# Kernel tuning notes

Measured on AMD Instinct MI355X. Metric: run time of the kernel, lower is better.

The kernel has to match this reference:

```python
import jax, jax.numpy as jnp
import numpy as np

N, E, B, IN, H = 20000, 50000, 1024, 32, 64

def setup_inputs() -> dict:
    key = jax.random.key(0)
    ks = jax.random.split(key, 32)
    d = {}
    d["x"] = jax.random.normal(ks[0], (N, IN), jnp.float32)
    d["edge_index"] = jax.random.randint(ks[1], (2, E), 0, N)
    d["edge_attr"] = jax.random.uniform(ks[2], (E, 6), dtype=jnp.float32)
    d["batch"] = jnp.sort(jax.random.randint(ks[3], (N,), 0, B))
    d["t"] = jax.random.uniform(ks[4], (B, 1), dtype=jnp.float32)
    d["p"] = jax.random.uniform(ks[5], (B, 1), dtype=jnp.float32)
    d["num_graphs"] = B
    def lin(k, fan_in, shape):
        return jax.random.normal(k, shape, jnp.float32) * (1.0 / np.sqrt(fan_in))
    # lin0: IN -> H
    d["W0"] = lin(ks[6], IN, (IN, H)); d["b0"] = jnp.zeros((H,), jnp.float32)
    # edge MLP: 6 -> 64 -> H*H
    d["We1"] = lin(ks[7], 6, (6, 64)); d["be1"] = jnp.zeros((64,), jnp.float32)
    d["We2"] = lin(ks[8], 64, (64, H * H)); d["be2"] = jnp.zeros((H * H,), jnp.float32)
    # NNConv root weight + bias
    d["Wroot"] = lin(ks[9], H, (H, H)); d["bconv"] = jnp.zeros((H,), jnp.float32)
    # GRU (input H, hidden H), torch layout [3H, *] gate order r,z,n
    d["gru_wih"] = lin(ks[10], H, (3 * H, H)); d["gru_whh"] = lin(ks[11], H, (3 * H, H))
    d["gru_bih"] = jnp.zeros((3 * H,), jnp.float32); d["gru_bhh"] = jnp.zeros((3 * H,), jnp.float32)
    # Set2Set LSTM (input 2H, hidden H), torch layout [4H, *] gate order i,f,g,o
    d["l_wih"] = lin(ks[12], 2 * H, (4 * H, 2 * H)); d["l_whh"] = lin(ks[13], H, (4 * H, H))
    d["l_bih"] = jnp.zeros((4 * H,), jnp.float32); d["l_bhh"] = jnp.zeros((4 * H,), jnp.float32)
    # readout MLP
    d["W1"] = lin(ks[14], 2 * H + 2, (2 * H + 2, H)); d["b1"] = jnp.zeros((H,), jnp.float32)
    d["W2"] = lin(ks[15], H, (H, 64)); d["b2"] = jnp.zeros((64,), jnp.float32)
    d["W3"] = lin(ks[16], 64, (64, 1)); d["b3"] = jnp.zeros((1,), jnp.float32)
    return d


def reference(x, edge_attr, t, p, W0, b0, We1, be1, We2, be2, Wroot, bconv,
              gru_wih, gru_whh, gru_bih, gru_bhh, l_wih, l_whh, l_bih, l_bhh,
              W1, b1, W2, b2, W3, b3, edge_index, batch, num_graphs):
    n_nodes = x.shape[0]
    hdim = W0.shape[1]
    src, dst = edge_index[0], edge_index[1]

    out = jax.nn.relu(x @ W0 + b0)            # [N,H]
    h = out

    # edge MLP -> per-edge weight matrices [E,H,H] (edge_attr is loop-invariant)
    ew = (jax.nn.relu(edge_attr @ We1 + be1) @ We2 + be2).reshape(-1, hdim, hdim)

    for _ in range(4):
        # NNConv: gather source features, per-edge matmul, scatter-add to targets
        msg = jnp.einsum('eh,eho->eo', out[src], ew)                 # [E,H]
        agg = jax.ops.segment_sum(msg, dst, num_segments=n_nodes)    # [N,H]
        m = jax.nn.relu(agg + out @ Wroot + bconv)
        # GRU step (single timestep)
        gi = m @ gru_wih.T + gru_bih
        gh = h @ gru_whh.T + gru_bhh
        ir, iz, inn = jnp.split(gi, 3, axis=-1)
        hr, hz, hn = jnp.split(gh, 3, axis=-1)
        r = jax.nn.sigmoid(ir + hr)
        z = jax.nn.sigmoid(iz + hz)
        nn_ = jnp.tanh(inn + r * hn)
        h = (1.0 - z) * nn_ + z * h
        out = h

    # Set2Set pooling, 3 processing steps
    qh = jnp.zeros((num_graphs, hdim), x.dtype)
    qc = jnp.zeros((num_graphs, hdim), x.dtype)
    q_star = jnp.zeros((num_graphs, 2 * hdim), x.dtype)
    for _ in range(3):
        g = q_star @ l_wih.T + l_bih + qh @ l_whh.T + l_bhh
        gi_, gf_, gg_, go_ = jnp.split(g, 4, axis=-1)
        qc = jax.nn.sigmoid(gf_) * qc + jax.nn.sigmoid(gi_) * jnp.tanh(gg_)
        qh = jax.nn.sigmoid(go_) * jnp.tanh(qc)
        q = qh                                                        # [B,H]
        e = jnp.sum(out * q[batch], axis=-1, keepdims=True)          # [N,1]
        emax = jax.ops.segment_max(e, batch, num_segments=num_graphs)
        a = jnp.exp(e - emax[batch])
        asum = jax.ops.segment_sum(a, batch, num_segments=num_graphs)
        a = a / asum[batch]                                           # segment softmax
        r_ = jax.ops.segment_sum(a * out, batch, num_segments=num_graphs)
        q_star = jnp.concatenate([q, r_], axis=-1)

    feat = jnp.concatenate([q_star, t, p], axis=-1)                   # [B,2H+2]
    y = jax.nn.relu(feat @ W1 + b1)
    y = jax.nn.relu(y @ W2 + b2)
    y = y @ W3 + b3
    return y.reshape(-1)
```

## Files before the change

### kernel.cpp

```cpp
#include <hip/hip_runtime.h>
#include <math.h>

#define N_NODES 20000
#define N_EDGES 50000
#define NB      1024
#define IND     32
#define HDIM    64

typedef __attribute__((ext_vector_type(8))) short bf16x8;
typedef __attribute__((ext_vector_type(4))) float f32x4;

static inline size_t align_up(size_t x, size_t a) { return (x + a - 1) & ~(a - 1); }

__device__ __forceinline__ float sigmoidf_(float x) {
    return 1.0f / (1.0f + __expf(-x));
}
__device__ __forceinline__ float tanhf_(float x) {
    float xc = fminf(fmaxf(x, -15.0f), 15.0f);
    float e = __expf(2.0f * xc);
    return (e - 1.0f) / (e + 1.0f);
}
__device__ __forceinline__ unsigned pk2(float p0, float p1) {
    unsigned u0 = __float_as_uint(p0) + 0x8000u;
    unsigned u1 = __float_as_uint(p1) + 0x8000u;
    return __builtin_amdgcn_perm(u1, u0, 0x07060302u);
}
__device__ __forceinline__ unsigned bf1(float v) {
    return (__float_as_uint(v) + 0x8000u) >> 16;
}

__global__ void k_transpose(const float* __restrict__ in, float* __restrict__ out, int R, int C) {
    int idx = blockIdx.x * 256 + threadIdx.x;
    if (idx >= R * C) return;
    int r = idx / C, c = idx - r * C;
    out[c * R + r] = in[idx];
}

__global__ void k_we2b(const float* __restrict__ We2, const float* __restrict__ be2,
                       short* __restrict__ We2b) {
    int idx = blockIdx.x * 256 + threadIdx.x;
    int s = idx >> 12;
    int col = idx & 4095;
    int k = col >> 6, o = col & 63;
    float val = (s < 64) ? We2[k * 4096 + s * 64 + o] : be2[k * 64 + o];
    int dst = s * 4096 + (((o >> 4) * 128 + (k >> 5) * 64 + ((k >> 3) & 3) * 16 + (o & 15)) << 3) + (k & 7);
    We2b[dst] = (short)bf1(val);
}

__global__ void k_wsplit(const float* __restrict__ Wroot, const float* __restrict__ gwhh,
                         const float* __restrict__ gwih,
                         short* __restrict__ WB1h, short* __restrict__ WB1l,
                         short* __restrict__ WB2h, short* __restrict__ WB2l) {
    int idx = blockIdx.x * 256 + threadIdx.x;
    if (idx >= 28672) return;
    bool b1 = idx < 16384;
    int li = b1 ? idx : idx - 16384;
    int j = li & 7, lane = (li >> 3) & 63, c = (li >> 9) & 1, otile = li >> 10;
    int k = c * 32 + (lane >> 4) * 8 + j;
    int o = otile * 16 + (lane & 15);
    float val;
    if (b1) val = (o < 64) ? Wroot[k * 64 + o] : gwhh[(o - 64) * 64 + k];
    else    val = gwih[o * 64 + k];
    unsigned hs = bf1(val);
    float lo = val - __uint_as_float(hs << 16);
    unsigned ls = bf1(lo);
    if (b1) { WB1h[li] = (short)hs; WB1l[li] = (short)ls; }
    else    { WB2h[li] = (short)hs; WB2l[li] = (short)ls; }
}

__global__ void k_offsets(const int* __restrict__ batch, int* __restrict__ offs) {
    int i = blockIdx.x * 256 + threadIdx.x;
    if (i > NB) return;
    int lo = 0, hi = N_NODES;
    while (lo < hi) { int mid = (lo + hi) >> 1; if (batch[mid] < i) lo = mid + 1; else hi = mid; }
    offs[i] = lo;
}

__global__ void k_count(const int* __restrict__ ei, int* __restrict__ deg) {
    int e = blockIdx.x * 256 + threadIdx.x;
    if (e < N_EDGES) atomicAdd(&deg[ei[N_EDGES + e]], 1);
}

__global__ void k_scan(const int* __restrict__ deg, int* __restrict__ rowptr, int* __restrict__ cursor) {
    __shared__ int s_w[16];
    int t = threadIdx.x;
    int base = t * 20;
    int v[20]; int s = 0;
#pragma unroll
    for (int i = 0; i < 20; ++i) {
        int idx = base + i;
        v[i] = (idx < N_NODES) ? deg[idx] : 0;
        s += v[i];
    }
    int lane = t & 63, w = t >> 6;
    int inc = s;
#pragma unroll
    for (int off = 1; off < 64; off <<= 1) {
        int o = __shfl_up(inc, off);
        if (lane >= off) inc += o;
    }
    if (lane == 63) s_w[w] = inc;
    __syncthreads();
    if (w == 0 && lane < 16) {
        int x = s_w[lane];
        int xs = x;
#pragma unroll
        for (int off = 1; off < 16; off <<= 1) {
            int o = __shfl_up(xs, off);
            if (lane >= off) xs += o;
        }
        s_w[lane] = xs - x;
    }
    __syncthreads();
    int run = s_w[w] + (inc - s);
#pragma unroll
    for (int i = 0; i < 20; ++i) {
        int idx = base + i;
        if (idx < N_NODES) { rowptr[idx] = run; cursor[idx] = run; }
        else if (idx == N_NODES) rowptr[idx] = run;
        run += v[i];
    }
}

__global__ void k_fill(const int* __restrict__ ei, int* __restrict__ cursor, int* __restrict__ perm) {
    int e = blockIdx.x * 256 + threadIdx.x;
    if (e < N_EDGES) {
        int pos = atomicAdd(&cursor[ei[N_EDGES + e]], 1);
        perm[pos] = e;
    }
}

__global__ void k_node_init(const float* __restrict__ x, const float* __restrict__ W0,
                            const float* __restrict__ b0, float* __restrict__ hbuf) {
    int tid = threadIdx.x;
    int w = tid >> 6, j = tid & 63;
    int n = blockIdx.x * 4 + w;
    float acc = b0[j];
    const float* xr = x + n * IND;
#pragma unroll
    for (int i = 0; i < IND; ++i) acc = fmaf(xr[i], W0[i * 64 + j], acc);
    hbuf[n * 64 + j] = fmaxf(acc, 0.0f);
}

__global__ void k_edge_feat(const float* __restrict__ ea, const float* __restrict__ We1,
                            const float* __restrict__ be1, float* __restrict__ re) {
    int tid = threadIdx.x;
    int w = tid >> 6, k = tid & 63;
    int e = blockIdx.x * 4 + w;
    if (e >= N_EDGES) return;
    float acc = be1[k];
    const float* er = ea + e * 6;
#pragma unroll
    for (int i = 0; i < 6; ++i) acc = fmaf(er[i], We1[i * 64 + k], acc);
    re[e * 64 + k] = fmaxf(acc, 0.0f);
}

__launch_bounds__(256, 3)
__global__ void k_msg_mfma(const float* __restrict__ hbuf, const float* __restrict__ reb,
                           const short* __restrict__ We2b, const int* __restrict__ ei,
                           float* __restrict__ msg) {
    __shared__ float s_v[64][64];
    int tid = threadIdx.x;
    int eb = blockIdx.x * 64;
    int lane = tid & 63;
    int w = tid >> 6;
    int l15 = lane & 15, lhi = lane >> 4;

    {
        int se = tid >> 2;
        int sh = tid & 3;
        int ge = eb + se;
        const float* rowp = (ge < N_EDGES) ? (hbuf + (size_t)ei[ge] * 64) : (const float*)0;
#pragma unroll
        for (int rr4 = 0; rr4 < 4; ++rr4) {
            int hb = rr4 * 16 + sh * 4;
            float4 vv = rowp ? *(const float4*)(rowp + hb) : make_float4(0.f, 0.f, 0.f, 0.f);
            s_v[hb + 0][se] = vv.x; s_v[hb + 1][se] = vv.y;
            s_v[hb + 2][se] = vv.z; s_v[hb + 3][se] = vv.w;
        }
    }

    union U { int4 i4; bf16x8 v; };
    U a_re[4][2];
#pragma unroll
    for (int m = 0; m < 4; ++m) {
        int ge = eb + m * 16 + l15;
        if (ge < N_EDGES) {
            const float* rp = reb + (size_t)ge * 64 + lhi * 8;
            float4 x0 = *(const float4*)(rp);
            float4 x1 = *(const float4*)(rp + 4);
            float4 y0 = *(const float4*)(rp + 32);
            float4 y1 = *(const float4*)(rp + 36);
            a_re[m][0].i4 = make_int4(pk2(x0.x, x0.y), pk2(x0.z, x0.w), pk2(x1.x, x1.y), pk2(x1.z, x1.w));
            a_re[m][1].i4 = make_int4(pk2(y0.x, y0.y), pk2(y0.z, y0.w), pk2(y1.x, y1.y), pk2(y1.z, y1.w));
        } else {
            a_re[m][0].i4 = make_int4(0, 0, 0, 0);
            a_re[m][1].i4 = make_int4(0, 0, 0, 0);
        }
    }

    const int4* bp0 = (const int4*)We2b + (w * 128 + lane);
    const int4* bp1 = bp0 + 64;
    int4 Sc0[4], Sc1[4];
#pragma unroll
    for (int j = 0; j < 4; ++j) {
        Sc0[j] = bp0[j * 512];
        Sc1[j] = bp1[j * 512];
    }

    __syncthreads();

    const f32x4 zero4 = {0.f, 0.f, 0.f, 0.f};
    f32x4 macc[4];
#pragma unroll
    for (int m = 0; m < 4; ++m) macc[m] = zero4;

    float4 vv[4], vn[4];
#pragma unroll
    for (int m = 0; m < 4; ++m) vv[m] = *(const float4*)&s_v[0][m * 16 + lhi * 4];

    for (int g = 0; g < 16; ++g) {
#pragma unroll
        for (int j = 0; j < 4; ++j) {
            int s = g * 4 + j;
            int snext = (s < 63) ? (s + 1) : 63;
#pragma unroll
            for (int m = 0; m < 4; ++m)
                vn[m] = *(const float4*)&s_v[snext][m * 16 + lhi * 4];
            U bb0, bb1; bb0.i4 = Sc0[j]; bb1.i4 = Sc1[j];
#pragma unroll
            for (int m = 0; m < 4; ++m) {
                f32x4 t = __builtin_amdgcn_mfma_f32_16x16x32_bf16(a_re[m][0].v, bb0.v, zero4, 0, 0, 0);
                t = __builtin_amdgcn_mfma_f32_16x16x32_bf16(a_re[m][1].v, bb1.v, t, 0, 0, 0);
                macc[m][0] = fmaf(vv[m].x, t[0], macc[m][0]);
                macc[m][1] = fmaf(vv[m].y, t[1], macc[m][1]);
                macc[m][2] = fmaf(vv[m].z, t[2], macc[m][2]);
                macc[m][3] = fmaf(vv[m].w, t[3], macc[m][3]);
            }
            int sload = (s + 4 <= 64) ? (s + 4) : 64;
            Sc0[j] = bp0[sload * 512];
            Sc1[j] = bp1[sload * 512];
#pragma unroll
            for (int m = 0; m < 4; ++m) vv[m] = vn[m];
        }
    }

    {
        U bb0, bb1; bb0.i4 = Sc0[0]; bb1.i4 = Sc1[0];
#pragma unroll
        for (int m = 0; m < 4; ++m) {
            int e = m * 16 + l15;
            U a0, a1;
            a0.i4 = make_int4(
                pk2(s_v[lhi * 8 + 0][e], s_v[lhi * 8 + 1][e]),
                pk2(s_v[lhi * 8 + 2][e], s_v[lhi * 8 + 3][e]),
                pk2(s_v[lhi * 8 + 4][e], s_v[lhi * 8 + 5][e]),
                pk2(s_v[lhi * 8 + 6][e], s_v[lhi * 8 + 7][e]));
            a1.i4 = make_int4(
                pk2(s_v[32 + lhi * 8 + 0][e], s_v[32 + lhi * 8 + 1][e]),
                pk2(s_v[32 + lhi * 8 + 2][e], s_v[32 + lhi * 8 + 3][e]),
                pk2(s_v[32 + lhi * 8 + 4][e], s_v[32 + lhi * 8 + 5][e]),
                pk2(s_v[32 + lhi * 8 + 6][e], s_v[32 + lhi * 8 + 7][e]));
            macc[m] = __builtin_amdgcn_mfma_f32_16x16x32_bf16(a0.v, bb0.v, macc[m], 0, 0, 0);
            macc[m] = __builtin_amdgcn_mfma_f32_16x16x32_bf16(a1.v, bb1.v, macc[m], 0, 0, 0);
        }
    }
    int o = w * 16 + l15;
#pragma unroll
    for (int m = 0; m < 4; ++m) {
#pragma unroll
        for (int r = 0; r < 4; ++r) {
            int el = m * 16 + lhi * 4 + r;
            int ge = eb + el;
            if (ge < N_EDGES) msg[(size_t)ge * 64 + o] = macc[m][r];
        }
    }
}

__launch_bounds__(256, 2)
__global__ void k_node_update(float* __restrict__ hbuf, const float* __restrict__ msg,
                              const int* __restrict__ rowptr, const int* __restrict__ perm,
                              const short* __restrict__ WB1h, const short* __restrict__ WB1l,
                              const short* __restrict__ WB2h, const short* __restrict__ WB2l,
                              const float* __restrict__ bconv, const float* __restrict__ bih,
                              const float* __restrict__ bhh) {
    __shared__ short s_hh[64][72];
    __shared__ short s_hl[64][72];
    __shared__ short s_mh[64][72];
    __shared__ short s_ml[64][72];
    __shared__ float s_agg[64][68];
    int tid = threadIdx.x;
    int nbase = blockIdx.x * 64;
    int lane = tid & 63, w = tid >> 6;
    int l15 = lane & 15, lhi = lane >> 4;

    {
        int nt = tid >> 2, q = tid & 3;
        int n = nbase + nt;
        bool valid = n < N_NODES;
#pragma unroll
        for (int c4 = 0; c4 < 4; ++c4) {
            int col = q * 16 + c4 * 4;
            float4 v = valid ? *(const float4*)&hbuf[(size_t)n * 64 + col]
                             : make_float4(0.f, 0.f, 0.f, 0.f);
            unsigned h01 = pk2(v.x, v.y), h23 = pk2(v.z, v.w);
            float f0 = __uint_as_float(h01 << 16);
            float f1 = __uint_as_float(h01 & 0xffff0000u);
            float f2 = __uint_as_float(h23 << 16);
            float f3 = __uint_as_float(h23 & 0xffff0000u);
            unsigned l01 = pk2(v.x - f0, v.y - f1), l23 = pk2(v.z - f2, v.w - f3);
            *(unsigned*)&s_hh[nt][col]     = h01;
            *(unsigned*)&s_hh[nt][col + 2] = h23;
            *(unsigned*)&s_hl[nt][col]     = l01;
            *(unsigned*)&s_hl[nt][col + 2] = l23;
        }
        float4 aggv[4];
#pragma unroll
        for (int c4 = 0; c4 < 4; ++c4)
            aggv[c4] = valid ? *(const float4*)&bconv[q * 16 + c4 * 4]
                             : make_float4(0.f, 0.f, 0.f, 0.f);
        if (valid) {
            int rs = rowptr[n], rend = rowptr[n + 1];
            for (int qq = rs; qq < rend; ++qq) {
                const float* mrow = msg + (size_t)perm[qq] * 64 + q * 16;
#pragma unroll
                for (int c4 = 0; c4 < 4; ++c4) {
                    float4 mv = *(const float4*)&mrow[c4 * 4];
                    aggv[c4].x += mv.x; aggv[c4].y += mv.y;
                    aggv[c4].z += mv.z; aggv[c4].w += mv.w;
                }
            }
        }
#pragma unroll
        for (int c4 = 0; c4 < 4; ++c4)
            *(float4*)&s_agg[nt][q * 16 + c4 * 4] = aggv[c4];
    }
    __syncthreads();

    union U { int4 i4; bf16x8 v; };
    U ah[4][2], al[4][2];
#pragma unroll
    for (int m = 0; m < 4; ++m)
#pragma unroll
        for (int c = 0; c < 2; ++c) {
            ah[m][c].i4 = *(const int4*)&s_hh[m * 16 + l15][c * 32 + lhi * 8];
            al[m][c].i4 = *(const int4*)&s_hl[m * 16 + l15][c * 32 + lhi * 8];
        }

    const int4* B1h = (const int4*)WB1h;
    const int4* B1l = (const int4*)WB1l;
    const int4* B2h = (const int4*)WB2h;
    const int4* B2l = (const int4*)WB2l;

    f32x4 C0[4], G[3][4], I[3][4];

    {
        int ot = w;
        U bh0, bh1, bl0, bl1;
        bh0.i4 = B1h[(ot * 2 + 0) * 64 + lane];
        bh1.i4 = B1h[(ot * 2 + 1) * 64 + lane];
        bl0.i4 = B1l[(ot * 2 + 0) * 64 + lane];
        bl1.i4 = B1l[(ot * 2 + 1) * 64 + lane];
#pragma unroll
        for (int m = 0; m < 4; ++m) {
            f32x4 c;
#pragma unroll
            for (int r = 0; r < 4; ++r) c[r] = s_agg[m * 16 + lhi * 4 + r][w * 16 + l15];
            c = __builtin_amdgcn_mfma_f32_16x16x32_bf16(ah[m][0].v, bh0.v, c, 0, 0, 0);
            c = __builtin_amdgcn_mfma_f32_16x16x32_bf16(ah[m][1].v, bh1.v, c, 0, 0, 0);
            c = __builtin_amdgcn_mfma_f32_16x16x32_bf16(al[m][0].v, bh0.v, c, 0, 0, 0);
            c = __builtin_amdgcn_mfma_f32_16x16x32_bf16(al[m][1].v, bh1.v, c, 0, 0, 0);
            c = __builtin_amdgcn_mfma_f32_16x16x32_bf16(ah[m][0].v, bl0.v, c, 0, 0, 0);
            c = __builtin_amdgcn_mfma_f32_16x16x32_bf16(ah[m][1].v, bl1.v, c, 0, 0, 0);
            C0[m] = c;
        }
    }
#pragma unroll
    for (int m = 0; m < 4; ++m)
#pragma unroll
        for (int r = 0; r < 4; ++r) {
            float mv = fmaxf(C0[m][r], 0.0f);
            int row = m * 16 + lhi * 4 + r, col = w * 16 + l15;
            unsigned hs = bf1(mv);
            float lof = mv - __uint_as_float(hs << 16);
            s_mh[row][col] = (short)hs;
            s_ml[row][col] = (short)bf1(lof);
        }
#pragma unroll
    for (int p = 1; p < 4; ++p) {
        int ot = p * 4 + w;
        U bh0, bh1, bl0, bl1;
        bh0.i4 = B1h[(ot * 2 + 0) * 64 + lane];
        bh1.i4 = B1h[(ot * 2 + 1) * 64 + lane];
        bl0.i4 = B1l[(ot * 2 + 0) * 64 + lane];
        bl1.i4 = B1l[(ot * 2 + 1) * 64 + lane];
        float bv = bhh[(p - 1) * 64 + w * 16 + l15];
#pragma unroll
        for (int m = 0; m < 4; ++m) {
            f32x4 c = {bv, bv, bv, bv};
            c = __builtin_amdgcn_mfma_f32_16x16x32_bf16(ah[m][0].v, bh0.v, c, 0, 0, 0);
            c = __builtin_amdgcn_mfma_f32_16x16x32_bf16(ah[m][1].v, bh1.v, c, 0, 0, 0);
            c = __builtin_amdgcn_mfma_f32_16x16x32_bf16(al[m][0].v, bh0.v, c, 0, 0, 0);
            c = __builtin_amdgcn_mfma_f32_16x16x32_bf16(al[m][1].v, bh1.v, c, 0, 0, 0);
            c = __builtin_amdgcn_mfma_f32_16x16x32_bf16(ah[m][0].v, bl0.v, c, 0, 0, 0);
            c = __builtin_amdgcn_mfma_f32_16x16x32_bf16(ah[m][1].v, bl1.v, c, 0, 0, 0);
            G[p - 1][m] = c;
        }
    }
    __syncthreads();
    U mh[4][2], ml[4][2];
#pragma unroll
    for (int m = 0; m < 4; ++m)
#pragma unroll
        for (int c = 0; c < 2; ++c) {
            mh[m][c].i4 = *(const int4*)&s_mh[m * 16 + l15][c * 32 + lhi * 8];
            ml[m][c].i4 = *(const int4*)&s_ml[m * 16 + l15][c * 32 + lhi * 8];
        }
#pragma unroll
    for (int p = 0; p < 3; ++p) {
        int ot = p * 4 + w;
        U bh0, bh1, bl0, bl1;
        bh0.i4 = B2h[(ot * 2 + 0) * 64 + lane];
        bh1.i4 = B2h[(ot * 2 + 1) * 64 + lane];
        bl0.i4 = B2l[(ot * 2 + 0) * 64 + lane];
        bl1.i4 = B2l[(ot * 2 + 1) * 64 + lane];
        float bv = bih[p * 64 + w * 16 + l15];
#pragma unroll
        for (int m = 0; m < 4; ++m) {
            f32x4 c = {bv, bv, bv, bv};
            c = __builtin_amdgcn_mfma_f32_16x16x32_bf16(mh[m][0].v, bh0.v, c, 0, 0, 0);
            c = __builtin_amdgcn_mfma_f32_16x16x32_bf16(mh[m][1].v, bh1.v, c, 0, 0, 0);
            c = __builtin_amdgcn_mfma_f32_16x16x32_bf16(ml[m][0].v, bh0.v, c, 0, 0, 0);
            c = __builtin_amdgcn_mfma_f32_16x16x32_bf16(ml[m][1].v, bh1.v, c, 0, 0, 0);
            c = __builtin_amdgcn_mfma_f32_16x16x32_bf16(mh[m][0].v, bl0.v, c, 0, 0, 0);
            c = __builtin_amdgcn_mfma_f32_16x16x32_bf16(mh[m][1].v, bl1.v, c, 0, 0, 0);
            I[p][m] = c;
        }
    }
#pragma unroll
    for (int m = 0; m < 4; ++m)
#pragma unroll
        for (int r = 0; r < 4; ++r) {
            int row = m * 16 + lhi * 4 + r;
            int n = nbase + row;
            if (n < N_NODES) {
                int col = w * 16 + l15;
                float hold = __uint_as_float(((unsigned)(unsigned short)s_hh[row][col]) << 16)
                           + __uint_as_float(((unsigned)(unsigned short)s_hl[row][col]) << 16);
                float rg = sigmoidf_(I[0][m][r] + G[0][m][r]);
                float z  = sigmoidf_(I[1][m][r] + G[1][m][r]);
                float nn = tanhf_(I[2][m][r] + rg * G[2][m][r]);
                hbuf[(size_t)n * 64 + col] = (1.0f - z) * nn + z * hold;
            }
        }
}

__global__ void k_lstm(const float* __restrict__ q_star, float* __restrict__ qh, float* __restrict__ qc,
                       const float* __restrict__ l_wihT, const float* __restrict__ l_whhT,
                       const float* __restrict__ l_bih, const float* __restrict__ l_bhh) {
    __shared__ float s_qs[128];
    __shared__ float s_qh[64];
    __shared__ float s_g[256];
    int b = blockIdx.x;
    int j = threadIdx.x;
    if (j < 128) s_qs[j] = q_star[b * 128 + j];
    else if (j < 192) s_qh[j - 128] = qh[b * 64 + (j - 128)];
    __syncthreads();
    float g = l_bih[j] + l_bhh[j];
#pragma unroll 8
    for (int i = 0; i < 128; ++i) g = fmaf(s_qs[i], l_wihT[i * 256 + j], g);
#pragma unroll 8
    for (int i = 0; i < 64; ++i)  g = fmaf(s_qh[i], l_whhT[i * 256 + j], g);
    s_g[j] = g;
    __syncthreads();
    if (j < 64) {
        float ci = sigmoidf_(s_g[j]);
        float cf = sigmoidf_(s_g[64 + j]);
        float cg = tanhf_(s_g[128 + j]);
        float co = sigmoidf_(s_g[192 + j]);
        float c = cf * qc[b * 64 + j] + ci * cg;
        qc[b * 64 + j] = c;
        qh[b * 64 + j] = co * tanhf_(c);
    }
}

__global__ void k_attention(const float* __restrict__ hbuf, const float* __restrict__ qh,
                            const int* __restrict__ offs, float* __restrict__ q_star) {
    int tid = threadIdx.x;
    int w = tid >> 6, lane = tid & 63;
    int b = blockIdx.x * 4 + w;
    int s = offs[b], e = offs[b + 1];
    float qv = qh[b * 64 + lane];
    float mx = -1e30f, l = 0.0f, racc = 0.0f;
    for (int n = s; n < e; ++n) {
        float xv = hbuf[n * 64 + lane];
        float prod = xv * qv;
#pragma unroll
        for (int off = 32; off > 0; off >>= 1) prod += __shfl_xor(prod, off);
        float mnew = fmaxf(mx, prod);
        float scale = __expf(mx - mnew);
        float wgt = __expf(prod - mnew);
        l = l * scale + wgt;
        racc = racc * scale + wgt * xv;
        mx = mnew;
    }
    float r = (e > s) ? (racc / l) : 0.0f;
    q_star[b * 128 + lane] = qv;
    q_star[b * 128 + 64 + lane] = r;
}

__global__ void k_readout(const float* __restrict__ q_star, const float* __restrict__ t,
                          const float* __restrict__ p, const float* __restrict__ W1,
                          const float* __restrict__ b1, const float* __restrict__ W2,
                          const float* __restrict__ b2, const float* __restrict__ W3,
                          const float* __restrict__ b3, float* __restrict__ y) {
    __shared__ float s_qs[4][128];
    __shared__ float s_y[4][64];
    int tid = threadIdx.x;
    int w = tid >> 6, j = tid & 63;
    int b = blockIdx.x * 4 + w;
    s_qs[w][j] = q_star[b * 128 + j];
    s_qs[w][64 + j] = q_star[b * 128 + 64 + j];
    __syncthreads();
    float acc = b1[j];
#pragma unroll 8
    for (int i = 0; i < 128; ++i) acc = fmaf(s_qs[w][i], W1[i * 64 + j], acc);
    acc = fmaf(t[b], W1[128 * 64 + j], acc);
    acc = fmaf(p[b], W1[129 * 64 + j], acc);
    acc = fmaxf(acc, 0.0f);
    s_y[w][j] = acc;
    __syncthreads();
    float acc2 = b2[j];
#pragma unroll 8
    for (int i = 0; i < 64; ++i) acc2 = fmaf(s_y[w][i], W2[i * 64 + j], acc2);
    acc2 = fmaxf(acc2, 0.0f);
    float part = acc2 * W3[j];
#pragma unroll
    for (int off = 32; off > 0; off >>= 1) part += __shfl_xor(part, off);
    if (j == 0) y[b] = part + b3[0];
}

extern "C" void kernel_launch(void* const* d_in, const int* in_sizes, int n_in,
                              void* d_out, int out_size, void* d_ws, size_t ws_size,
                              hipStream_t stream) {
    const float* x     = (const float*)d_in[0];
    const int*   ei    = (const int*)  d_in[1];
    const float* ea    = (const float*)d_in[2];
    const int*   batch = (const int*)  d_in[3];
    const float* t     = (const float*)d_in[4];
    const float* p     = (const float*)d_in[5];
    const float* W0    = (const float*)d_in[7];
    const float* b0    = (const float*)d_in[8];
    const float* We1   = (const float*)d_in[9];
    const float* be1   = (const float*)d_in[10];
    const float* We2   = (const float*)d_in[11];
    const float* be2   = (const float*)d_in[12];
    const float* Wroot = (const float*)d_in[13];
    const float* bconv = (const float*)d_in[14];
    const float* gwih  = (const float*)d_in[15];
    const float* gwhh  = (const float*)d_in[16];
    const float* gbih  = (const float*)d_in[17];
    const float* gbhh  = (const float*)d_in[18];
    const float* lwih  = (const float*)d_in[19];
    const float* lwhh  = (const float*)d_in[20];
    const float* lbih  = (const float*)d_in[21];
    const float* lbhh  = (const float*)d_in[22];
    const float* W1    = (const float*)d_in[23];
    const float* b1    = (const float*)d_in[24];
    const float* W2    = (const float*)d_in[25];
    const float* b2    = (const float*)d_in[26];
    const float* W3    = (const float*)d_in[27];
    const float* b3    = (const float*)d_in[28];
    float* y = (float*)d_out;

    char* ws = (char*)d_ws;
    size_t off = 0;
    auto alloc = [&](size_t nbytes) {
        void* ptr = (void*)(ws + off);
        off += align_up(nbytes, 256);
        return ptr;
    };
    float* hbuf   = (float*)alloc((size_t)N_NODES * 64 * 4);
    float* reb    = (float*)alloc((size_t)N_EDGES * 64 * 4);
    float* msg    = (float*)alloc((size_t)N_EDGES * 64 * 4);
    short* We2b   = (short*)alloc((size_t)65 * 4096 * 2);
    short* WB1h   = (short*)alloc(16384 * 2);
    short* WB1l   = (short*)alloc(16384 * 2);
    short* WB2h   = (short*)alloc(12288 * 2);
    short* WB2l   = (short*)alloc(12288 * 2);
    float* lwihT  = (float*)alloc(128 * 256 * 4);
    float* lwhhT  = (float*)alloc(64 * 256 * 4);
    float* qh     = (float*)alloc(NB * 64 * 4);
    float* qc     = (float*)alloc(NB * 64 * 4);
    float* qstar  = (float*)alloc(NB * 128 * 4);
    int*   offs   = (int*)  alloc((NB + 1) * 4);
    int*   deg    = (int*)  alloc(N_NODES * 4);
    int*   rowptr = (int*)  alloc((N_NODES + 1) * 4);
    int*   cursor = (int*)  alloc(N_NODES * 4);
    int*   perm   = (int*)  alloc(N_EDGES * 4);

    k_transpose<<<(256 * 128 + 255) / 256, 256, 0, stream>>>(lwih, lwihT, 256, 128);
    k_transpose<<<(256 * 64 + 255) / 256, 256, 0, stream>>>(lwhh, lwhhT, 256, 64);
    k_we2b<<<65 * 4096 / 256, 256, 0, stream>>>(We2, be2, We2b);
    k_wsplit<<<(28672 + 255) / 256, 256, 0, stream>>>(Wroot, gwhh, gwih, WB1h, WB1l, WB2h, WB2l);
    k_offsets<<<5, 256, 0, stream>>>(batch, offs);
    hipMemsetAsync(qh, 0, (size_t)(NB * 64 + NB * 64 + NB * 128) * 4, stream);
    hipMemsetAsync(deg, 0, (size_t)N_NODES * 4, stream);
    k_count<<<(N_EDGES + 255) / 256, 256, 0, stream>>>(ei, deg);
    k_scan<<<1, 1024, 0, stream>>>(deg, rowptr, cursor);
    k_fill<<<(N_EDGES + 255) / 256, 256, 0, stream>>>(ei, cursor, perm);

    k_node_init<<<N_NODES / 4, 256, 0, stream>>>(x, W0, b0, hbuf);
    k_edge_feat<<<N_EDGES / 4, 256, 0, stream>>>(ea, We1, be1, reb);

    for (int it = 0; it < 4; ++it) {
        k_msg_mfma<<<(N_EDGES + 63) / 64, 256, 0, stream>>>(hbuf, reb, We2b, ei, msg);
        k_node_update<<<(N_NODES + 63) / 64, 256, 0, stream>>>(hbuf, msg, rowptr, perm,
                                                               WB1h, WB1l, WB2h, WB2l,
                                                               bconv, gbih, gbhh);
    }

    for (int itr = 0; itr < 3; ++itr) {
        k_lstm<<<NB, 256, 0, stream>>>(qstar, qh, qc, lwihT, lwhhT, lbih, lbhh);
        k_attention<<<NB / 4, 256, 0, stream>>>(hbuf, qh, offs, qstar);
    }

    k_readout<<<NB / 4, 256, 0, stream>>>(qstar, t, p, W1, b1, W2, b2, W3, b3, y);
}
```

Baseline: 490.7 us.

## Fuse prep, init and Set2Set kernels; widen message kernel to 128 edges

The weight-prep, transpose and offset kernels are merged into one launch, and the node-init and edge-feature kernels into another. The three LSTM/attention rounds and the readout become a single per-graph kernel that keeps the LSTM state in registers, so the qh, qc and q_star buffers and their memset go away. The message MFMA kernel now uses 512 threads covering 128 edges per block, with two edge halves sharing output tiles and a shorter weight prefetch depth. The aim is fewer launches and less global traffic, at the cost of a serial per-graph Set2Set kernel with only 64 threads per block and different occupancy in the message kernel.

```diff
diff --git a/kernel.cpp b/kernel.cpp
--- a/kernel.cpp
+++ b/kernel.cpp
@@ -29,51 +29,57 @@
     return (__float_as_uint(v) + 0x8000u) >> 16;
 }
 
-__global__ void k_transpose(const float* __restrict__ in, float* __restrict__ out, int R, int C) {
-    int idx = blockIdx.x * 256 + threadIdx.x;
-    if (idx >= R * C) return;
-    int r = idx / C, c = idx - r * C;
-    out[c * R + r] = in[idx];
-}
-
-__global__ void k_we2b(const float* __restrict__ We2, const float* __restrict__ be2,
-                       short* __restrict__ We2b) {
-    int idx = blockIdx.x * 256 + threadIdx.x;
-    int s = idx >> 12;
-    int col = idx & 4095;
-    int k = col >> 6, o = col & 63;
-    float val = (s < 64) ? We2[k * 4096 + s * 64 + o] : be2[k * 64 + o];
-    int dst = s * 4096 + (((o >> 4) * 128 + (k >> 5) * 64 + ((k >> 3) & 3) * 16 + (o & 15)) << 3) + (k & 7);
-    We2b[dst] = (short)bf1(val);
-}
-
-__global__ void k_wsplit(const float* __restrict__ Wroot, const float* __restrict__ gwhh,
-                         const float* __restrict__ gwih,
-                         short* __restrict__ WB1h, short* __restrict__ WB1l,
-                         short* __restrict__ WB2h, short* __restrict__ WB2l) {
-    int idx = blockIdx.x * 256 + threadIdx.x;
-    if (idx >= 28672) return;
-    bool b1 = idx < 16384;
-    int li = b1 ? idx : idx - 16384;
-    int j = li & 7, lane = (li >> 3) & 63, c = (li >> 9) & 1, otile = li >> 10;
-    int k = c * 32 + (lane >> 4) * 8 + j;
-    int o = otile * 16 + (lane & 15);
-    float val;
-    if (b1) val = (o < 64) ? Wroot[k * 64 + o] : gwhh[(o - 64) * 64 + k];
-    else    val = gwih[o * 64 + k];
-    unsigned hs = bf1(val);
-    float lo = val - __uint_as_float(hs << 16);
-    unsigned ls = bf1(lo);
-    if (b1) { WB1h[li] = (short)hs; WB1l[li] = (short)ls; }
-    else    { WB2h[li] = (short)hs; WB2l[li] = (short)ls; }
-}
-
-__global__ void k_offsets(const int* __restrict__ batch, int* __restrict__ offs) {
-    int i = blockIdx.x * 256 + threadIdx.x;
-    if (i > NB) return;
-    int lo = 0, hi = N_NODES;
-    while (lo < hi) { int mid = (lo + hi) >> 1; if (batch[mid] < i) lo = mid + 1; else hi = mid; }
-    offs[i] = lo;
+__global__ void k_prep(const float* __restrict__ We2, const float* __restrict__ be2,
+                       short* __restrict__ We2b,
+                       const float* __restrict__ Wroot, const float* __restrict__ gwhh,
+                       const float* __restrict__ gwih,
+                       short* __restrict__ WB1h, short* __restrict__ WB1l,
+                       short* __restrict__ WB2h, short* __restrict__ WB2l,
+                       const float* __restrict__ lwih, const float* __restrict__ lwhh,
+                       float* __restrict__ lwihP, float* __restrict__ lwhhP,
+                       const int* __restrict__ batch, int* __restrict__ offs) {
+    int bid = blockIdx.x, tid = threadIdx.x;
+    if (bid < 1040) {
+        int idx = bid * 256 + tid;
+        int s = idx >> 12;
+        int col = idx & 4095;
+        int k = col >> 6, o = col & 63;
+        float val = (s < 64) ? We2[k * 4096 + s * 64 + o] : be2[k * 64 + o];
+        int dst = s * 4096 + (((o >> 4) * 128 + (k >> 5) * 64 + ((k >> 3) & 3) * 16 + (o & 15)) << 3) + (k & 7);
+        We2b[dst] = (short)bf1(val);
+    } else if (bid < 1152) {
+        int idx = (bid - 1040) * 256 + tid;
+        if (idx < 28672) {
+            bool b1 = idx < 16384;
+            int li = b1 ? idx : idx - 16384;
+            int j = li & 7, lane = (li >> 3) & 63, c = (li >> 9) & 1, otile = li >> 10;
+            int k = c * 32 + (lane >> 4) * 8 + j;
+            int o = otile * 16 + (lane & 15);
+            float val;
+            if (b1) val = (o < 64) ? Wroot[k * 64 + o] : gwhh[(o - 64) * 64 + k];
+            else    val = gwih[o * 64 + k];
+            unsigned hs = bf1(val);
+            float lo = val - __uint_as_float(hs << 16);
+            unsigned ls = bf1(lo);
+            if (b1) { WB1h[li] = (short)hs; WB1l[li] = (short)ls; }
+            else    { WB2h[li] = (short)hs; WB2l[li] = (short)ls; }
+        }
+    } else if (bid < 1280) {
+        int idx = (bid - 1152) * 256 + tid;
+        int g = idx & 3, j = (idx >> 2) & 63, i = idx >> 8;
+        lwihP[idx] = lwih[(g * 64 + j) * 128 + i];
+    } else if (bid < 1344) {
+        int idx = (bid - 1280) * 256 + tid;
+        int g = idx & 3, j = (idx >> 2) & 63, i = idx >> 8;
+        lwhhP[idx] = lwhh[(g * 64 + j) * 64 + i];
+    } else {
+        int i = (bid - 1344) * 256 + tid;
+        if (i <= NB) {
+            int lo = 0, hi = N_NODES;
+            while (lo < hi) { int mid = (lo + hi) >> 1; if (batch[mid] < i) lo = mid + 1; else hi = mid; }
+            offs[i] = lo;
+        }
+    }
 }
 
 __global__ void k_count(const int* __restrict__ ei, int* __restrict__ deg) {
@@ -130,40 +136,43 @@
     }
 }
 
-__global__ void k_node_init(const float* __restrict__ x, const float* __restrict__ W0,
-                            const float* __restrict__ b0, float* __restrict__ hbuf) {
+__global__ void k_init_feat(const float* __restrict__ x, const float* __restrict__ W0,
+                            const float* __restrict__ b0, float* __restrict__ hbuf,
+                            const float* __restrict__ ea, const float* __restrict__ We1,
+                            const float* __restrict__ be1, float* __restrict__ re) {
+    int bid = blockIdx.x;
     int tid = threadIdx.x;
     int w = tid >> 6, j = tid & 63;
-    int n = blockIdx.x * 4 + w;
-    float acc = b0[j];
-    const float* xr = x + n * IND;
-#pragma unroll
-    for (int i = 0; i < IND; ++i) acc = fmaf(xr[i], W0[i * 64 + j], acc);
-    hbuf[n * 64 + j] = fmaxf(acc, 0.0f);
-}
-
-__global__ void k_edge_feat(const float* __restrict__ ea, const float* __restrict__ We1,
-                            const float* __restrict__ be1, float* __restrict__ re) {
-    int tid = threadIdx.x;
-    int w = tid >> 6, k = tid & 63;
-    int e = blockIdx.x * 4 + w;
-    if (e >= N_EDGES) return;
-    float acc = be1[k];
-    const float* er = ea + e * 6;
-#pragma unroll
-    for (int i = 0; i < 6; ++i) acc = fmaf(er[i], We1[i * 64 + k], acc);
-    re[e * 64 + k] = fmaxf(acc, 0.0f);
-}
-
-__launch_bounds__(256, 3)
+    if (bid < 5000) {
+        int n = bid * 4 + w;
+        float acc = b0[j];
+        const float* xr = x + n * IND;
+#pragma unroll
+        for (int i = 0; i < IND; ++i) acc = fmaf(xr[i], W0[i * 64 + j], acc);
+        hbuf[n * 64 + j] = fmaxf(acc, 0.0f);
+    } else {
+        int e = (bid - 5000) * 4 + w;
+        if (e >= N_EDGES) return;
+        float acc = be1[j];
+        const float* er = ea + e * 6;
+#pragma unroll
+        for (int i = 0; i < 6; ++i) acc = fmaf(er[i], We1[i * 64 + j], acc);
+        re[e * 64 + j] = fmaxf(acc, 0.0f);
+    }
+}
+
+__launch_bounds__(512, 4)
 __global__ void k_msg_mfma(const float* __restrict__ hbuf, const float* __restrict__ reb,
                            const short* __restrict__ We2b, const int* __restrict__ ei,
                            float* __restrict__ msg) {
-    __shared__ float s_v[64][64];
+    __shared__ float s_v[64][128];
     int tid = threadIdx.x;
-    int eb = blockIdx.x * 64;
+    int eb = blockIdx.x * 128;
     int lane = tid & 63;
     int w = tid >> 6;
+    int half = w >> 2;
+    int ot = w & 3;
+    int ebase = half * 64;
     int l15 = lane & 15, lhi = lane >> 4;
 
     {
@@ -184,7 +193,7 @@
     U a_re[4][2];
 #pragma unroll
     for (int m = 0; m < 4; ++m) {
-        int ge = eb + m * 16 + l15;
+        int ge = eb + ebase + m * 16 + l15;
         if (ge < N_EDGES) {
             const float* rp = reb + (size_t)ge * 64 + lhi * 8;
             float4 x0 = *(const float4*)(rp);
@@ -199,11 +208,11 @@
         }
     }
 
-    const int4* bp0 = (const int4*)We2b + (w * 128 + lane);
+    const int4* bp0 = (const int4*)We2b + (ot * 128 + lane);
     const int4* bp1 = bp0 + 64;
-    int4 Sc0[4], Sc1[4];
-#pragma unroll
-    for (int j = 0; j < 4; ++j) {
+    int4 Sc0[2], Sc1[2];
+#pragma unroll
+    for (int j = 0; j < 2; ++j) {
         Sc0[j] = bp0[j * 512];
         Sc1[j] = bp1[j * 512];
     }
@@ -217,16 +226,16 @@
 
     float4 vv[4], vn[4];
 #pragma unroll
-    for (int m = 0; m < 4; ++m) vv[m] = *(const float4*)&s_v[0][m * 16 + lhi * 4];
-
-    for (int g = 0; g < 16; ++g) {
-#pragma unroll
-        for (int j = 0; j < 4; ++j) {
-            int s = g * 4 + j;
+    for (int m = 0; m < 4; ++m) vv[m] = *(const float4*)&s_v[0][ebase + m * 16 + lhi * 4];
+
+    for (int g = 0; g < 32; ++g) {
+#pragma unroll
+        for (int j = 0; j < 2; ++j) {
+            int s = g * 2 + j;
             int snext = (s < 63) ? (s + 1) : 63;
 #pragma unroll
             for (int m = 0; m < 4; ++m)
-                vn[m] = *(const float4*)&s_v[snext][m * 16 + lhi * 4];
+                vn[m] = *(const float4*)&s_v[snext][ebase + m * 16 + lhi * 4];
             U bb0, bb1; bb0.i4 = Sc0[j]; bb1.i4 = Sc1[j];
 #pragma unroll
             for (int m = 0; m < 4; ++m) {
@@ -237,7 +246,7 @@
                 macc[m][2] = fmaf(vv[m].z, t[2], macc[m][2]);
                 macc[m][3] = fmaf(vv[m].w, t[3], macc[m][3]);
             }
-            int sload = (s + 4 <= 64) ? (s + 4) : 64;
+            int sload = (s + 2 <= 64) ? (s + 2) : 64;
             Sc0[j] = bp0[sload * 512];
             Sc1[j] = bp1[sload * 512];
 #pragma unroll
@@ -249,7 +258,7 @@
         U bb0, bb1; bb0.i4 = Sc0[0]; bb1.i4 = Sc1[0];
 #pragma unroll
         for (int m = 0; m < 4; ++m) {
-            int e = m * 16 + l15;
+            int e = ebase + m * 16 + l15;
             U a0, a1;
             a0.i4 = make_int4(
                 pk2(s_v[lhi * 8 + 0][e], s_v[lhi * 8 + 1][e]),
@@ -265,12 +274,12 @@
             macc[m] = __builtin_amdgcn_mfma_f32_16x16x32_bf16(a1.v, bb1.v, macc[m], 0, 0, 0);
         }
     }
-    int o = w * 16 + l15;
+    int o = ot * 16 + l15;
 #pragma unroll
     for (int m = 0; m < 4; ++m) {
 #pragma unroll
         for (int r = 0; r < 4; ++r) {
-            int el = m * 16 + lhi * 4 + r;
+            int el = ebase + m * 16 + lhi * 4 + r;
             int ge = eb + el;
             if (ge < N_EDGES) msg[(size_t)ge * 64 + o] = macc[m][r];
         }
@@ -455,84 +464,83 @@
         }
 }
 
-__global__ void k_lstm(const float* __restrict__ q_star, float* __restrict__ qh, float* __restrict__ qc,
-                       const float* __restrict__ l_wihT, const float* __restrict__ l_whhT,
-                       const float* __restrict__ l_bih, const float* __restrict__ l_bhh) {
-    __shared__ float s_qs[128];
-    __shared__ float s_qh[64];
-    __shared__ float s_g[256];
+__launch_bounds__(64)
+__global__ void k_set2set(const float* __restrict__ hbuf, const int* __restrict__ offs,
+                          const float* __restrict__ t, const float* __restrict__ p,
+                          const float* __restrict__ lwihP, const float* __restrict__ lwhhP,
+                          const float* __restrict__ l_bih, const float* __restrict__ l_bhh,
+                          const float* __restrict__ W1, const float* __restrict__ b1,
+                          const float* __restrict__ W2, const float* __restrict__ b2,
+                          const float* __restrict__ W3, const float* __restrict__ b3,
+                          float* __restrict__ y) {
+    __shared__ float s_qs[192];
+    __shared__ float s_y[64];
     int b = blockIdx.x;
     int j = threadIdx.x;
-    if (j < 128) s_qs[j] = q_star[b * 128 + j];
-    else if (j < 192) s_qh[j - 128] = qh[b * 64 + (j - 128)];
-    __syncthreads();
-    float g = l_bih[j] + l_bhh[j];
+    int s = offs[b], e = offs[b + 1];
+    float qh = 0.f, qc = 0.f, qs0 = 0.f, qs1 = 0.f;
+    float bi0 = l_bih[j]       + l_bhh[j];
+    float bi1 = l_bih[64 + j]  + l_bhh[64 + j];
+    float bi2 = l_bih[128 + j] + l_bhh[128 + j];
+    float bi3 = l_bih[192 + j] + l_bhh[192 + j];
+
+    for (int iter = 0; iter < 3; ++iter) {
+        s_qs[j] = qs0; s_qs[64 + j] = qs1; s_qs[128 + j] = qh;
+        __syncthreads();
+        float g0 = bi0, g1 = bi1, g2 = bi2, g3 = bi3;
 #pragma unroll 8
-    for (int i = 0; i < 128; ++i) g = fmaf(s_qs[i], l_wihT[i * 256 + j], g);
+        for (int i = 0; i < 128; ++i) {
+            float qsv = s_qs[i];
+            float4 wv = *(const float4*)&lwihP[(i * 64 + j) * 4];
+            g0 = fmaf(qsv, wv.x, g0);
+            g1 = fmaf(qsv, wv.y, g1);
+            g2 = fmaf(qsv, wv.z, g2);
+            g3 = fmaf(qsv, wv.w, g3);
+        }
 #pragma unroll 8
-    for (int i = 0; i < 64; ++i)  g = fmaf(s_qh[i], l_whhT[i * 256 + j], g);
-    s_g[j] = g;
-    __syncthreads();
-    if (j < 64) {
-        float ci = sigmoidf_(s_g[j]);
-        float cf = sigmoidf_(s_g[64 + j]);
-        float cg = tanhf_(s_g[128 + j]);
-        float co = sigmoidf_(s_g[192 + j]);
-        float c = cf * qc[b * 64 + j] + ci * cg;
-        qc[b * 64 + j] = c;
-        qh[b * 64 + j] = co * tanhf_(c);
-    }
-}
-
-__global__ void k_attention(const float* __restrict__ hbuf, const float* __restrict__ qh,
-                            const int* __restrict__ offs, float* __restrict__ q_star) {
-    int tid = threadIdx.x;
-    int w = tid >> 6, lane = tid & 63;
-    int b = blockIdx.x * 4 + w;
-    int s = offs[b], e = offs[b + 1];
-    float qv = qh[b * 64 + lane];
-    float mx = -1e30f, l = 0.0f, racc = 0.0f;
-    for (int n = s; n < e; ++n) {
-        float xv = hbuf[n * 64 + lane];
-        float prod = xv * qv;
-#pragma unroll
-        for (int off = 32; off > 0; off >>= 1) prod += __shfl_xor(prod, off);
-        float mnew = fmaxf(mx, prod);
-        float scale = __expf(mx - mnew);
-        float wgt = __expf(prod - mnew);
-        l = l * scale + wgt;
-        racc = racc * scale + wgt * xv;
-        mx = mnew;
-    }
-    float r = (e > s) ? (racc / l) : 0.0f;
-    q_star[b * 128 + lane] = qv;
-    q_star[b * 128 + 64 + lane] = r;
-}
-
-__global__ void k_readout(const float* __restrict__ q_star, const float* __restrict__ t,
-                          const float* __restrict__ p, const float* __restrict__ W1,
-                          const float* __restrict__ b1, const float* __restrict__ W2,
-                          const float* __restrict__ b2, const float* __restrict__ W3,
-                          const float* __restrict__ b3, float* __restrict__ y) {
-    __shared__ float s_qs[4][128];
-    __shared__ float s_y[4][64];
-    int tid = threadIdx.x;
-    int w = tid >> 6, j = tid & 63;
-    int b = blockIdx.x * 4 + w;
-    s_qs[w][j] = q_star[b * 128 + j];
-    s_qs[w][64 + j] = q_star[b * 128 + 64 + j];
+        for (int i = 0; i < 64; ++i) {
+            float qhv = s_qs[128 + i];
+            float4 wv = *(const float4*)&lwhhP[(i * 64 + j) * 4];
+            g0 = fmaf(qhv, wv.x, g0);
+            g1 = fmaf(qhv, wv.y, g1);
+            g2 = fmaf(qhv, wv.z, g2);
+            g3 = fmaf(qhv, wv.w, g3);
+        }
+        __syncthreads();
+        float ci = sigmoidf_(g0), cf = sigmoidf_(g1);
+        float cg = tanhf_(g2),   co = sigmoidf_(g3);
+        qc = cf * qc + ci * cg;
+        qh = co * tanhf_(qc);
+        float qv = qh;
+        float mx = -1e30f, l = 0.0f, racc = 0.0f;
+        for (int n = s; n < e; ++n) {
+            float xv = hbuf[(size_t)n * 64 + j];
+            float prod = xv * qv;
+#pragma unroll
+            for (int off = 32; off > 0; off >>= 1) prod += __shfl_xor(prod, off);
+            float mnew = fmaxf(mx, prod);
+            float scale = __expf(mx - mnew);
+            float wgt = __expf(prod - mnew);
+            l = l * scale + wgt;
+            racc = racc * scale + wgt * xv;
+            mx = mnew;
+        }
+        float r = (e > s) ? (racc / l) : 0.0f;
+        qs0 = qv; qs1 = r;
+    }
+    s_qs[j] = qs0; s_qs[64 + j] = qs1;
     __syncthreads();
     float acc = b1[j];
 #pragma unroll 8
-    for (int i = 0; i < 128; ++i) acc = fmaf(s_qs[w][i], W1[i * 64 + j], acc);
+    for (int i = 0; i < 128; ++i) acc = fmaf(s_qs[i], W1[i * 64 + j], acc);
     acc = fmaf(t[b], W1[128 * 64 + j], acc);
     acc = fmaf(p[b], W1[129 * 64 + j], acc);
     acc = fmaxf(acc, 0.0f);
-    s_y[w][j] = acc;
+    s_y[j] = acc;
     __syncthreads();
     float acc2 = b2[j];
 #pragma unroll 8
-    for (int i = 0; i < 64; ++i) acc2 = fmaf(s_y[w][i], W2[i * 64 + j], acc2);
+    for (int i = 0; i < 64; ++i) acc2 = fmaf(s_y[i], W2[i * 64 + j], acc2);
     acc2 = fmaxf(acc2, 0.0f);
     float part = acc2 * W3[j];
 #pragma unroll
@@ -588,42 +596,31 @@
     short* WB1l   = (short*)alloc(16384 * 2);
     short* WB2h   = (short*)alloc(12288 * 2);
     short* WB2l   = (short*)alloc(12288 * 2);
-    float* lwihT  = (float*)alloc(128 * 256 * 4);
-    float* lwhhT  = (float*)alloc(64 * 256 * 4);
-    float* qh     = (float*)alloc(NB * 64 * 4);
-    float* qc     = (float*)alloc(NB * 64 * 4);
-    float* qstar  = (float*)alloc(NB * 128 * 4);
+    float* lwihP  = (float*)alloc(32768 * 4);
+    float* lwhhP  = (float*)alloc(16384 * 4);
     int*   offs   = (int*)  alloc((NB + 1) * 4);
     int*   deg    = (int*)  alloc(N_NODES * 4);
     int*   rowptr = (int*)  alloc((N_NODES + 1) * 4);
     int*   cursor = (int*)  alloc(N_NODES * 4);
     int*   perm   = (int*)  alloc(N_EDGES * 4);
 
-    k_transpose<<<(256 * 128 + 255) / 256, 256, 0, stream>>>(lwih, lwihT, 256, 128);
-    k_transpose<<<(256 * 64 + 255) / 256, 256, 0, stream>>>(lwhh, lwhhT, 256, 64);
-    k_we2b<<<65 * 4096 / 256, 256, 0, stream>>>(We2, be2, We2b);
-    k_wsplit<<<(28672 + 255) / 256, 256, 0, stream>>>(Wroot, gwhh, gwih, WB1h, WB1l, WB2h, WB2l);
-    k_offsets<<<5, 256, 0, stream>>>(batch, offs);
-    hipMemsetAsync(qh, 0, (size_t)(NB * 64 + NB * 64 + NB * 128) * 4, stream);
+    k_prep<<<1349, 256, 0, stream>>>(We2, be2, We2b, Wroot, gwhh, gwih,
+                                     WB1h, WB1l, WB2h, WB2l,
+                                     lwih, lwhh, lwihP, lwhhP, batch, offs);
     hipMemsetAsync(deg, 0, (size_t)N_NODES * 4, stream);
     k_count<<<(N_EDGES + 255) / 256, 256, 0, stream>>>(ei, deg);
     k_scan<<<1, 1024, 0, stream>>>(deg, rowptr, cursor);
     k_fill<<<(N_EDGES + 255) / 256, 256, 0, stream>>>(ei, cursor, perm);
 
-    k_node_init<<<N_NODES / 4, 256, 0, stream>>>(x, W0, b0, hbuf);
-    k_edge_feat<<<N_EDGES / 4, 256, 0, stream>>>(ea, We1, be1, reb);
+    k_init_feat<<<17500, 256, 0, stream>>>(x, W0, b0, hbuf, ea, We1, be1, reb);
 
     for (int it = 0; it < 4; ++it) {
-        k_msg_mfma<<<(N_EDGES + 63) / 64, 256, 0, stream>>>(hbuf, reb, We2b, ei, msg);
+        k_msg_mfma<<<(N_EDGES + 127) / 128, 512, 0, stream>>>(hbuf, reb, We2b, ei, msg);
         k_node_update<<<(N_NODES + 63) / 64, 256, 0, stream>>>(hbuf, msg, rowptr, perm,
                                                                WB1h, WB1l, WB2h, WB2l,
                                                                bconv, gbih, gbhh);
     }
 
-    for (int itr = 0; itr < 3; ++itr) {
-        k_lstm<<<NB, 256, 0, stream>>>(qstar, qh, qc, lwihT, lwhhT, lbih, lbhh);
-        k_attention<<<NB / 4, 256, 0, stream>>>(hbuf, qh, offs, qstar);
-    }
-
-    k_readout<<<NB / 4, 256, 0, stream>>>(qstar, t, p, W1, b1, W2, b2, W3, b3, y);
-}
+    k_set2set<<<NB, 64, 0, stream>>>(hbuf, offs, t, p, lwihP, lwhhP, lbih, lbhh,
+                                     W1, b1, W2, b2, W3, b3, y);
+}
```

New measurement: 528.4 us. 7.7% more time.
